# Kernel tuning notes

Measured on AMD Instinct MI355X. Metric: run time of the kernel, lower is better.

Reference implementation:

```python
import jax, jax.numpy as jnp
import numpy as np

LMAX = 6
F_IN, F_OUT = 64, 64
N_ROT = 64  # n_angles**3
IRREP_FLAT = sum((2 * l + 1) ** 2 for l in range(LMAX + 1))  # 455
BATCH = 1024


def setup_inputs() -> dict:
    key = jax.random.key(0)
    k_x, k_d, k_w = jax.random.split(key, 3)
    x = jax.random.normal(k_x, (BATCH, F_IN, IRREP_FLAT), dtype=jnp.float32)
    D = jax.random.normal(k_d, (N_ROT, IRREP_FLAT), dtype=jnp.float32)  # flat Wigner-D buffer
    w = jax.random.normal(k_w, (F_IN, F_OUT, N_ROT), dtype=jnp.float32)
    return {"x": x, "D": D, "w": w}


def reference(x, D, w):
    B, f_in, _ = x.shape
    f_out = w.shape[1]
    n_rot = D.shape[0]
    # psi[f,g,i] = sum_n D[n,i] * w[f,g,n] / sqrt(N)
    psi = jnp.einsum('ni,fgn->fgi', D, w) / jnp.sqrt(jnp.asarray(n_rot, x.dtype))
    outs = []
    off = 0
    for l in range(LMAX + 1):
        d = 2 * l + 1          # irrep dim == multiplicity for so3_irreps
        blk = d * d
        # weight block: (f_in, f_out, mul_in=u, mul_out=v)
        Wl = psi[:, :, off:off + blk].reshape(f_in, f_out, d, d)
        # input block: (B, f_in, mul=u, irrep_dim=m)
        xl = x[:, :, off:off + blk].reshape(B, f_in, d, d)
        # e3nn Linear path norm ('element'): 1/sqrt(f_in * mul_in)
        norm = 1.0 / np.sqrt(f_in * d)
        yl = jnp.einsum('bfum,fguv->bgvm', xl, Wl) * norm
        outs.append(yl.reshape(B, f_out, blk))
        off += blk
    return jnp.concatenate(outs, axis=-1)  # (B, f_out, 455)
```

## Files before the change

kernel.cpp:

```cpp
#include <hip/hip_runtime.h>
#include <stdint.h>


typedef __bf16 bf16x8 __attribute__((ext_vector_type(8)));
typedef float floatx4 __attribute__((ext_vector_type(4)));

#define XROW 29120

__device__ __forceinline__ unsigned short f2bf(float f) {
  union { float f; unsigned int u; } c; c.f = f;
  unsigned int u = c.u;
  return (unsigned short)((u + 0x7FFFu + ((u >> 16) & 1u)) >> 16);
}
__device__ __forceinline__ unsigned int pack2(float a, float b) {
  return (unsigned int)f2bf(a) | ((unsigned int)f2bf(b) << 16);
}

__host__ __device__ constexpr int d_of(int L) { return 2 * L + 1; }
__host__ __device__ constexpr int off_of(int L) { int s = 0; for (int i = 0; i < L; ++i) s += d_of(i) * d_of(i); return s; }
__host__ __device__ constexpr size_t a_off(int L) { size_t s = 0; for (int i = 0; i < L; ++i) s += (size_t)65536 * d_of(i) * d_of(i); return s; }
__host__ __device__ constexpr size_t b_off(int L) { size_t s = a_off(7); for (int i = 0; i < L; ++i) s += (size_t)4096 * d_of(i) * (d_of(i) + 1); return s; }

__global__ __launch_bounds__(256) void prep(const float* __restrict__ x, const float* __restrict__ Dm,
                                            const float* __restrict__ w, unsigned short* __restrict__ ws) {
  __shared__ __align__(16) float smem[64 * 68 + 64 * 172];
  const int tid = threadIdx.x;
  const int bid = blockIdx.x;

  if (bid < 448) {
    float* wg = smem;
    float* Dl = smem + 64 * 68;
    const int g = bid & 63, l = bid >> 6;
    const int d = 2 * l + 1, d2 = d * d, K = 64 * d;
    int off = 0; size_t boff = a_off(7);
    for (int i = 0; i < l; ++i) { int dd = 2 * i + 1; off += dd * dd; boff += (size_t)4096 * dd * (dd + 1); }
    unsigned short* B = ws + boff;

    for (int t = tid; t < 4096; t += 256) {
      int n = t & 63, f = t >> 6;
      wg[n * 68 + f] = w[(size_t)f * 4096 + g * 64 + n];
    }
    for (int t = tid; t < 64 * 172; t += 256) {
      int n = t / 172, r = t - n * 172;
      Dl[t] = (r < d2) ? Dm[n * 455 + off + r] : 0.f;
    }
    __syncthreads();

    const float sl = 1.0f / (64.0f * sqrtf((float)d));
    const int RT = (d2 + 3) >> 2;
    for (int tt = tid; tt < 16 * RT; tt += 256) {
      const int ft = tt & 15, rt = tt >> 4;
      float acc[4][4] = {};
      for (int n = 0; n < 64; ++n) {
        floatx4 wv = *(const floatx4*)(wg + n * 68 + ft * 4);
        floatx4 dv = *(const floatx4*)(Dl + n * 172 + rt * 4);
#pragma unroll
        for (int a = 0; a < 4; ++a)
#pragma unroll
          for (int b2 = 0; b2 < 4; ++b2) acc[a][b2] += wv[a] * dv[b2];
      }
#pragma unroll
      for (int b2 = 0; b2 < 4; ++b2) {
        int r = rt * 4 + b2;
        if (r < d2) {
          int u = r / d, v = r - u * d;
          size_t base = (size_t)(g * d + v) * K + u * 64 + ft * 4;
#pragma unroll
          for (int a = 0; a < 4; ++a) B[base + a] = f2bf(acc[a][b2] * sl);
        }
      }
    }
    {
      int nn = 64 * d + g;
      for (int k = tid; k < K; k += 256) B[(size_t)nn * K + k] = 0;
    }
  } else {
    float* xs = smem;
    const int b = bid - 448;
    const float* xb = x + (size_t)b * XROW;
    size_t aoff = 0;

    for (int t = tid; t < 64 * 165; t += 256) { int f = t / 165, c = t - f * 165; xs[t] = xb[(size_t)f * 455 + c]; }
    __syncthreads();
    int off = 0;
#pragma unroll
    for (int l = 0; l < 5; ++l) {
      const int d = 2 * l + 1, d2 = d * d, n1 = 64 * d2;
      unsigned int* A = (unsigned int*)(ws + aoff + (size_t)b * n1);
      for (int t = tid; t < (n1 >> 1); t += 256) {
        int f2 = t & 31, s = t >> 5;
        int u = s % d, m = s / d;
        int c = off + u * d + m;
        A[t] = pack2(xs[(2 * f2) * 165 + c], xs[(2 * f2 + 1) * 165 + c]);
      }
      off += d2; aoff += (size_t)1024 * n1;
    }
    __syncthreads();
    for (int t = tid; t < 64 * 121; t += 256) { int f = t / 121, c = t - f * 121; xs[t] = xb[(size_t)f * 455 + 165 + c]; }
    __syncthreads();
    {
      const int n1 = 64 * 121;
      unsigned int* A = (unsigned int*)(ws + aoff + (size_t)b * n1);
      for (int t = tid; t < (n1 >> 1); t += 256) {
        int f2 = t & 31, s = t >> 5;
        int u = s % 11, m = s / 11;
        int c = u * 11 + m;
        A[t] = pack2(xs[(2 * f2) * 121 + c], xs[(2 * f2 + 1) * 121 + c]);
      }
      aoff += (size_t)1024 * n1;
    }
    __syncthreads();
    for (int t = tid; t < 64 * 169; t += 256) { int f = t / 169, c = t - f * 169; xs[t] = xb[(size_t)f * 455 + 286 + c]; }
    __syncthreads();
    {
      const int n1 = 64 * 169;
      unsigned int* A = (unsigned int*)(ws + aoff + (size_t)b * n1);
      for (int t = tid; t < (n1 >> 1); t += 256) {
        int f2 = t & 31, s = t >> 5;
        int u = s % 13, m = s / 13;
        int c = u * 13 + m;
        A[t] = pack2(xs[(2 * f2) * 169 + c], xs[(2 * f2 + 1) * 169 + c]);
      }
    }
  }
}

__device__ __forceinline__ void async_copy16(const void* gp, void* lp) {
  __builtin_amdgcn_global_load_lds((__attribute__((address_space(1))) void*)gp,
                                   (__attribute__((address_space(3))) void*)lp, 16, 0, 0);
}

template <int N>
__device__ __forceinline__ void wait_vmcnt() {
  asm volatile("s_waitcnt vmcnt(%0)" :: "n"(N) : "memory");
}

template <int L>
__device__ __forceinline__ void gemm_body(int local, const unsigned short* __restrict__ ws,
                                          float* __restrict__ out,
                                          unsigned short* As, unsigned short* Bs) {
  constexpr int d = 2 * L + 1;
  constexpr int K = 64 * d;
  constexpr int NT = (d + 1) / 2;
  constexpr int OFF = off_of(L);
  constexpr int KT = 2 * d;
  const unsigned short* A = ws + a_off(L);
  const unsigned short* B = ws + b_off(L);
  const int x4 = local & 3, tt = local >> 2;
  const int mt = (tt / NT) * 4 + x4;
  const int nt = tt % NT;
  const int tid = threadIdx.x;
  const int w = tid >> 6, ln = tid & 63;
  const int wm = w >> 1, wn = w & 1;
  const int q = ln >> 4, r16 = ln & 15;

  const unsigned short* gp[6];
  unsigned short* ldst[6];
#pragma unroll
  for (int i = 0; i < 6; ++i) {
    int c = i * 256 + tid;
    if (i < 4) {
      int row = c >> 2, ch = (c & 3) ^ ((c >> 3) & 3);
      gp[i] = A + (size_t)(mt * 256 + row) * K + ch * 8;
      ldst[i] = As + (i * 256 + w * 64) * 8;
    } else {
      int c2 = c - 1024;
      int row = c2 >> 2, ch = (c2 & 3) ^ ((c2 >> 3) & 3);
      gp[i] = B + (size_t)(nt * 128 + row) * K + ch * 8;
      ldst[i] = Bs + ((i - 4) * 256 + w * 64) * 8;
    }
  }

  const int sq = q ^ ((r16 >> 1) & 3);
  const int aoffs0 = (wm * 128 + r16) * 32 + sq * 8;
  const int boffs0 = (wn * 64 + r16) * 32 + sq * 8;

  floatx4 acc[8][4] = {};

#pragma unroll
  for (int t = 0; t < 2; ++t) {
    if (t < KT) {
#pragma unroll
      for (int i = 0; i < 6; ++i) { async_copy16(gp[i], ldst[i] + t * (i < 4 ? 8192 : 4096)); gp[i] += 32; }
    }
  }

#pragma unroll
  for (int kt = 0; kt < KT; ++kt) {
    if (kt < KT - 1) wait_vmcnt<6>();
    else             wait_vmcnt<0>();
    __builtin_amdgcn_s_barrier();
    __builtin_amdgcn_sched_barrier(0);

    const unsigned short* Asc = As + (kt % 3) * 8192;
    const unsigned short* Bsc = Bs + (kt % 3) * 4096;
    bf16x8 af[8], bfr[4];
#pragma unroll
    for (int mi = 0; mi < 8; ++mi) af[mi] = *(const bf16x8*)(Asc + aoffs0 + mi * 512);
#pragma unroll
    for (int ni = 0; ni < 4; ++ni) bfr[ni] = *(const bf16x8*)(Bsc + boffs0 + ni * 512);

    if (kt + 2 < KT) {
#pragma unroll
      for (int i = 0; i < 6; ++i) { async_copy16(gp[i], ldst[i] + ((kt + 2) % 3) * (i < 4 ? 8192 : 4096)); gp[i] += 32; }
    }

#pragma unroll
    for (int mi = 0; mi < 8; ++mi)
#pragma unroll
      for (int ni = 0; ni < 4; ++ni)
        acc[mi][ni] = __builtin_amdgcn_mfma_f32_16x16x32_bf16(af[mi], bfr[ni], acc[mi][ni], 0, 0, 0);
    __builtin_amdgcn_sched_barrier(0);
  }

#pragma unroll
  for (int ni = 0; ni < 4; ++ni) {
    int Cc = nt * 128 + wn * 64 + ni * 16 + r16;
    if (Cc < 64 * d) {
      int g = Cc / d, v = Cc - (Cc / d) * d;
#pragma unroll
      for (int mi = 0; mi < 8; ++mi) {
        int R0 = mt * 256 + wm * 128 + mi * 16 + q * 4;
#pragma unroll
        for (int reg = 0; reg < 4; ++reg) {
          int R = R0 + reg;
          int bb = R / d, m = R - (R / d) * d;
          out[(size_t)bb * XROW + g * 455 + OFF + v * d + m] = acc[mi][ni][reg];
        }
      }
    }
  }
}

__global__ __launch_bounds__(256, 2) void gemm_all(const unsigned short* __restrict__ ws, float* __restrict__ out) {
  __shared__ alignas(16) unsigned short As[3 * 256 * 32];
  __shared__ alignas(16) unsigned short Bs[3 * 128 * 32];
  int b0 = 1007 - (int)blockIdx.x;
  if      (b0 <    4) gemm_body<0>(b0,        ws, out, As, Bs);
  else if (b0 <   28) gemm_body<1>(b0 -    4, ws, out, As, Bs);
  else if (b0 <   88) gemm_body<2>(b0 -   28, ws, out, As, Bs);
  else if (b0 <  200) gemm_body<3>(b0 -   88, ws, out, As, Bs);
  else if (b0 <  380) gemm_body<4>(b0 -  200, ws, out, As, Bs);
  else if (b0 <  644) gemm_body<5>(b0 -  380, ws, out, As, Bs);
  else                gemm_body<6>(b0 -  644, ws, out, As, Bs);
}

extern "C" void kernel_launch(void* const* d_in, const int* in_sizes, int n_in,
                              void* d_out, int out_size, void* d_ws, size_t ws_size,
                              hipStream_t stream) {
  const float* x = (const float*)d_in[0];
  const float* D = (const float*)d_in[1];
  const float* w = (const float*)d_in[2];
  float* out = (float*)d_out;
  unsigned short* ws = (unsigned short*)d_ws;

  hipLaunchKernelGGL(prep, dim3(1472), dim3(256), 0, stream, x, D, w, ws);
  hipLaunchKernelGGL(gemm_all, dim3(1008), dim3(256), 0, stream, ws, out);
}
```

Baseline: 344.1 us.

## Restage x transpose by feature chunks with vectorized loads and shrink LDS

The x-repacking blocks now copy contiguous 24- or 20-feature slabs of the input row with 16-byte vector loads, instead of strided per-irrep column gathers. Each slab is then written as packed 4-feature bf16 groups (uint2 stores) for all seven irreps. The psi-precompute blocks now tile the D columns in chunks of 88, so shared memory drops from about 15.4K floats to 24*455. The goal is coalesced global reads, wider stores and more blocks resident per CU, at the cost of more barriers and 8-byte stores scattered across phases.

Result: slower. 364.5 us (+5.9%).

```diff
diff --git a/kernel.cpp b/kernel.cpp
--- a/kernel.cpp
+++ b/kernel.cpp
@@ -21,9 +21,30 @@
 __host__ __device__ constexpr size_t a_off(int L) { size_t s = 0; for (int i = 0; i < L; ++i) s += (size_t)65536 * d_of(i) * d_of(i); return s; }
 __host__ __device__ constexpr size_t b_off(int L) { size_t s = a_off(7); for (int i = 0; i < L; ++i) s += (size_t)4096 * d_of(i) * (d_of(i) + 1); return s; }
 
+template <int NQ, int Q0>
+__device__ __forceinline__ void store_phase(const float* __restrict__ xs, unsigned short* __restrict__ ws,
+                                            int b, int tid) {
+  int off = 0; size_t aoff = 0;
+#pragma unroll
+  for (int l = 0; l < 7; ++l) {
+    const int d = 2 * l + 1, d2 = d * d;
+    uint2* A2 = (uint2*)(ws + aoff) + (size_t)b * (16 * d2);
+    for (int t = tid; t < d2 * NQ; t += 256) {
+      int fq = t % NQ, s = t / NQ;
+      int u = s % d, m = s / d;
+      const float* xc = xs + off + u * d + m;
+      uint2 v;
+      v.x = pack2(xc[(4 * fq + 0) * 455], xc[(4 * fq + 1) * 455]);
+      v.y = pack2(xc[(4 * fq + 2) * 455], xc[(4 * fq + 3) * 455]);
+      A2[s * 16 + Q0 + fq] = v;
+    }
+    off += d2; aoff += (size_t)65536 * d2;
+  }
+}
+
 __global__ __launch_bounds__(256) void prep(const float* __restrict__ x, const float* __restrict__ Dm,
                                             const float* __restrict__ w, unsigned short* __restrict__ ws) {
-  __shared__ __align__(16) float smem[64 * 68 + 64 * 172];
+  __shared__ __align__(16) float smem[24 * 455];
   const int tid = threadIdx.x;
   const int bid = blockIdx.x;
 
@@ -40,33 +61,39 @@
       int n = t & 63, f = t >> 6;
       wg[n * 68 + f] = w[(size_t)f * 4096 + g * 64 + n];
     }
-    for (int t = tid; t < 64 * 172; t += 256) {
-      int n = t / 172, r = t - n * 172;
-      Dl[t] = (r < d2) ? Dm[n * 455 + off + r] : 0.f;
-    }
-    __syncthreads();
 
     const float sl = 1.0f / (64.0f * sqrtf((float)d));
-    const int RT = (d2 + 3) >> 2;
-    for (int tt = tid; tt < 16 * RT; tt += 256) {
-      const int ft = tt & 15, rt = tt >> 4;
-      float acc[4][4] = {};
-      for (int n = 0; n < 64; ++n) {
-        floatx4 wv = *(const floatx4*)(wg + n * 68 + ft * 4);
-        floatx4 dv = *(const floatx4*)(Dl + n * 172 + rt * 4);
-#pragma unroll
-        for (int a = 0; a < 4; ++a)
-#pragma unroll
-          for (int b2 = 0; b2 < 4; ++b2) acc[a][b2] += wv[a] * dv[b2];
+    for (int c0 = 0; c0 < d2; c0 += 88) {
+      __syncthreads();
+      for (int t = tid; t < 64 * 88; t += 256) {
+        int n = t / 88, rc = t - n * 88;
+        int r = c0 + rc;
+        Dl[t] = (r < d2) ? Dm[n * 455 + off + r] : 0.f;
       }
-#pragma unroll
-      for (int b2 = 0; b2 < 4; ++b2) {
-        int r = rt * 4 + b2;
-        if (r < d2) {
-          int u = r / d, v = r - u * d;
-          size_t base = (size_t)(g * d + v) * K + u * 64 + ft * 4;
-#pragma unroll
-          for (int a = 0; a < 4; ++a) B[base + a] = f2bf(acc[a][b2] * sl);
+      __syncthreads();
+
+      const int rem = d2 - c0;
+      const int RTc = ((rem > 88 ? 88 : rem) + 3) >> 2;
+      for (int tt = tid; tt < 16 * RTc; tt += 256) {
+        const int ft = tt & 15, rt = tt >> 4;
+        float acc[4][4] = {};
+        for (int n = 0; n < 64; ++n) {
+          floatx4 wv = *(const floatx4*)(wg + n * 68 + ft * 4);
+          floatx4 dv = *(const floatx4*)(Dl + n * 88 + rt * 4);
+#pragma unroll
+          for (int a = 0; a < 4; ++a)
+#pragma unroll
+            for (int b2 = 0; b2 < 4; ++b2) acc[a][b2] += wv[a] * dv[b2];
+        }
+#pragma unroll
+        for (int b2 = 0; b2 < 4; ++b2) {
+          int r = c0 + rt * 4 + b2;
+          if (r < d2) {
+            int u = r / d, v = r - u * d;
+            size_t base = (size_t)(g * d + v) * K + u * 64 + ft * 4;
+#pragma unroll
+            for (int a = 0; a < 4; ++a) B[base + a] = f2bf(acc[a][b2] * sl);
+          }
         }
       }
     }
@@ -78,50 +105,30 @@
     float* xs = smem;
     const int b = bid - 448;
     const float* xb = x + (size_t)b * XROW;
-    size_t aoff = 0;
-
-    for (int t = tid; t < 64 * 165; t += 256) { int f = t / 165, c = t - f * 165; xs[t] = xb[(size_t)f * 455 + c]; }
-    __syncthreads();
-    int off = 0;
-#pragma unroll
-    for (int l = 0; l < 5; ++l) {
-      const int d = 2 * l + 1, d2 = d * d, n1 = 64 * d2;
-      unsigned int* A = (unsigned int*)(ws + aoff + (size_t)b * n1);
-      for (int t = tid; t < (n1 >> 1); t += 256) {
-        int f2 = t & 31, s = t >> 5;
-        int u = s % d, m = s / d;
-        int c = off + u * d + m;
-        A[t] = pack2(xs[(2 * f2) * 165 + c], xs[(2 * f2 + 1) * 165 + c]);
-      }
-      off += d2; aoff += (size_t)1024 * n1;
-    }
-    __syncthreads();
-    for (int t = tid; t < 64 * 121; t += 256) { int f = t / 121, c = t - f * 121; xs[t] = xb[(size_t)f * 455 + 165 + c]; }
-    __syncthreads();
-    {
-      const int n1 = 64 * 121;
-      unsigned int* A = (unsigned int*)(ws + aoff + (size_t)b * n1);
-      for (int t = tid; t < (n1 >> 1); t += 256) {
-        int f2 = t & 31, s = t >> 5;
-        int u = s % 11, m = s / 11;
-        int c = u * 11 + m;
-        A[t] = pack2(xs[(2 * f2) * 121 + c], xs[(2 * f2 + 1) * 121 + c]);
-      }
-      aoff += (size_t)1024 * n1;
-    }
-    __syncthreads();
-    for (int t = tid; t < 64 * 169; t += 256) { int f = t / 169, c = t - f * 169; xs[t] = xb[(size_t)f * 455 + 286 + c]; }
-    __syncthreads();
-    {
-      const int n1 = 64 * 169;
-      unsigned int* A = (unsigned int*)(ws + aoff + (size_t)b * n1);
-      for (int t = tid; t < (n1 >> 1); t += 256) {
-        int f2 = t & 31, s = t >> 5;
-        int u = s % 13, m = s / 13;
-        int c = u * 13 + m;
-        A[t] = pack2(xs[(2 * f2) * 169 + c], xs[(2 * f2 + 1) * 169 + c]);
-      }
-    }
+
+    {
+      const floatx4* src = (const floatx4*)xb;
+      floatx4* dst = (floatx4*)xs;
+      for (int t = tid; t < 24 * 455 / 4; t += 256) dst[t] = src[t];
+    }
+    __syncthreads();
+    store_phase<6, 0>(xs, ws, b, tid);
+    __syncthreads();
+    {
+      const floatx4* src = (const floatx4*)(xb + 24 * 455);
+      floatx4* dst = (floatx4*)xs;
+      for (int t = tid; t < 20 * 455 / 4; t += 256) dst[t] = src[t];
+    }
+    __syncthreads();
+    store_phase<5, 6>(xs, ws, b, tid);
+    __syncthreads();
+    {
+      const floatx4* src = (const floatx4*)(xb + 44 * 455);
+      floatx4* dst = (floatx4*)xs;
+      for (int t = tid; t < 20 * 455 / 4; t += 256) dst[t] = src[t];
+    }
+    __syncthreads();
+    store_phase<5, 11>(xs, ws, b, tid);
   }
 }
 
```
